# Kernel tuning notes

Hardware: AMD Instinct MI355X
Metric: run time of the kernel (lower is better)

The kernel has to match this reference:

```python
import jax, jax.numpy as jnp
import numpy as np

SEQ_LEN = 256
NLAYERS = 3
H = 128  # latent_dim == input_dim
OUT_DIM = 2
BATCH = 1024


def setup_inputs() -> dict:
    key = jax.random.key(0)
    ks = jax.random.split(key, 7)
    s = 1.0 / np.sqrt(H)  # PyTorch RNN init scale
    return {
        "hiddens": jax.random.normal(ks[0], (BATCH, NLAYERS, H), jnp.float32),
        "W_ih": jax.random.uniform(ks[1], (NLAYERS, 3 * H, H), jnp.float32, -s, s),
        "W_hh": jax.random.uniform(ks[2], (NLAYERS, 3 * H, H), jnp.float32, -s, s),
        "b_ih": jax.random.uniform(ks[3], (NLAYERS, 3 * H), jnp.float32, -s, s),
        "b_hh": jax.random.uniform(ks[4], (NLAYERS, 3 * H), jnp.float32, -s, s),
        "fc_w": jax.random.uniform(ks[5], (OUT_DIM, H), jnp.float32, -s, s),
        "fc_b": jax.random.uniform(ks[6], (OUT_DIM,), jnp.float32, -s, s),
    }


def _gru_cell(x, h, w_ih, w_hh, bi, bh):
    # x, h: [B, H]; w_*: [3H, H]; b_*: [3H]; PyTorch gate order (r, z, n)
    gx = x @ w_ih.T + bi          # [B, 3H]
    gh = h @ w_hh.T + bh          # [B, 3H]
    xr, xz, xn = jnp.split(gx, 3, axis=-1)
    hr, hz, hn = jnp.split(gh, 3, axis=-1)
    r = jax.nn.sigmoid(xr + hr)
    z = jax.nn.sigmoid(xz + hz)
    n = jnp.tanh(xn + r * hn)
    return (1.0 - z) * n + z * h


def reference(hiddens, W_ih, W_hh, b_ih, b_hh, fc_w, fc_b):
    # hiddens: [B, L, H] -> layer-major [L, B, H] (torch transposes 0,1)
    h = jnp.transpose(hiddens, (1, 0, 2))
    B = hiddens.shape[0]
    x0 = jnp.zeros((B, H), hiddens.dtype)  # torch.zeros initial input

    def step(carry, _):
        x, h = carry
        new_h = []
        inp = x
        for l in range(NLAYERS):
            hl = _gru_cell(inp, h[l], W_ih[l], W_hh[l], b_ih[l], b_hh[l])
            new_h.append(hl)
            inp = hl  # top-layer output feeds next layer / next step
        return (inp, jnp.stack(new_h)), inp

    (_, _), outs = jax.lax.scan(step, (x0, h), None, length=SEQ_LEN)
    outs = jnp.transpose(outs, (1, 0, 2))        # [B, T, H]
    return outs @ fc_w.T + fc_b                  # [B, T, out_dim]
```

## Files before the change

kernel.cpp:

```cpp
#include <hip/hip_runtime.h>
#include <stdint.h>

typedef int   v4i __attribute__((ext_vector_type(4)));
typedef float v4f __attribute__((ext_vector_type(4)));

#define SLOT_SZ  13824
#define LO_OFF   6912
#define BIAS_OFF (2*SLOT_SZ)
#define FC_OFF   (BIAS_OFF + 6144)
#define SMEM_SZ  (FC_OFF + 2048)

#define QW   1436.84056f
#define C1f  4.38394754e-5f
#define C2f  3.45193507e-7f
#define L2E  1.44269504f
#define CR1  (-(L2E)*C1f)
#define CR2  (-(L2E)*C2f)
#define CX1  (2.0f*L2E*C1f)
#define CX2  (2.0f*L2E*C2f)

#define MFMA(A,B,C) __builtin_amdgcn_mfma_i32_16x16x64_i8(A, B, C, 0, 0, 0)

__global__ void prep_weights(const float* __restrict__ Wih,
                             const float* __restrict__ Whh,
                             int8_t* __restrict__ img) {
  int bid = blockIdx.x, lane = threadIdx.x;
  int w = bid / 36, blk = bid % 36;
  int l = blk / 12, rem = blk % 12, o = rem >> 1, kh = rem & 1;
  const float* M = (o & 1) ? Whh : Wih;
  int row = (o >> 1) * 128 + w * 16 + (lane & 15);
  int k0 = kh * 64 + (lane >> 4) * 16;
  const float* src = M + l * 49152 + row * 128 + k0;
  int words[4];
  #pragma unroll
  for (int j4 = 0; j4 < 4; ++j4) {
    unsigned wd = 0;
    #pragma unroll
    for (int j = 0; j < 4; ++j) {
      int q = (int)rintf(src[j4 * 4 + j] * QW);
      wd |= ((unsigned)(q & 255)) << (8 * j);
    }
    words[j4] = (int)wd;
  }
  *(v4i*)(img + (((long)bid) * 64 + lane) * 16) = *(const v4i*)words;
}

__global__ __launch_bounds__(512, 2)
void gru_main(const float* __restrict__ hiddens, const float* __restrict__ bih,
              const float* __restrict__ bhh, const float* __restrict__ fcw,
              const float* __restrict__ fcb, const int8_t* __restrict__ img,
              float* __restrict__ out) {
  extern __shared__ char smem[];
  const int tid = threadIdx.x, wg = blockIdx.x;
  const int lane = tid & 63, w = tid >> 6, col = lane & 15, q = lane >> 4;

  v4i wr[36];
  #pragma unroll
  for (int i = 0; i < 36; ++i)
    wr[i] = *(const v4i*)(img + (((long)(w * 36 + i)) * 64 + lane) * 16);

  if (tid < 128) {
    int kh = tid >> 6, ln = tid & 63, c2 = ln & 15, q2 = ln >> 4;
    int words[4] = {0, 0, 0, 0};
    if (c2 < 2) {
      const float* src = fcw + c2 * 128 + kh * 64 + q2 * 16;
      #pragma unroll
      for (int j4 = 0; j4 < 4; ++j4) {
        unsigned wd = 0;
        #pragma unroll
        for (int j = 0; j < 4; ++j) {
          int qv = (int)rintf(src[j4 * 4 + j] * QW);
          wd |= ((unsigned)(qv & 255)) << (8 * j);
        }
        words[j4] = (int)wd;
      }
    }
    *(v4i*)(smem + FC_OFF + kh * 1024 + ln * 16) = *(const v4i*)words;
  }
  for (int i = tid; i < 1536; i += 512) {
    int l = i >> 9, type = (i >> 7) & 3, h = i & 127;
    float bv;
    if      (type == 0) bv = -L2E * (bih[l * 384 + h]       + bhh[l * 384 + h]);
    else if (type == 1) bv = -L2E * (bih[l * 384 + 128 + h] + bhh[l * 384 + 128 + h]);
    else if (type == 2) bv = 2.0f * L2E * bih[l * 384 + 256 + h];
    else                bv = 2.0f * L2E * bhh[l * 384 + 256 + h];
    *(float*)(smem + BIAS_OFF + i * 4) = bv;
  }
  for (int i = tid; i < 6144; i += 512) {
    int l = i >> 11, b = (i >> 7) & 15, h = i & 127;
    float v = hiddens[((long)(wg * 16 + b)) * 384 + l * 128 + h];
    float f = v * 15.875f, fhi = rintf(f);
    *(int8_t*)(smem + l * 2304 + b * 144 + h)          = (int8_t)(int)fhi;
    *(int8_t*)(smem + l * 2304 + b * 144 + h + LO_OFF) = (int8_t)(int)rintf((f - fhi) * 127.f);
  }
  v4f hst[3];
  #pragma unroll
  for (int l = 0; l < 3; ++l)
    #pragma unroll
    for (int r = 0; r < 4; ++r)
      hst[l][r] = hiddens[((long)(wg * 16 + col)) * 384 + l * 128 + w * 16 + q * 4 + r];

  const float fcb0 = fcb[0], fcb1 = fcb[1];
  __syncthreads();

  const char* fragb = smem + col * 144 + q * 16;
  char* ewb = smem + col * 144 + w * 16 + q * 4;
  const char* biasb = smem + BIAS_OFF + (w * 16 + q * 4) * 4;

  v4i c2h[2], c2l[2];

  #pragma unroll 1
  for (int t = 0; t < 256; ++t) {
    const int so = (t & 1) * SLOT_SZ;
    const int sn = SLOT_SZ - so;
    #pragma unroll
    for (int l = 0; l < 3; ++l) {
      v4f bRv = *(const v4f*)(biasb + (l * 4 + 0) * 512);
      v4f bZv = *(const v4f*)(biasb + (l * 4 + 1) * 512);
      v4f bXv = *(const v4f*)(biasb + (l * 4 + 2) * 512);
      v4f bHv = *(const v4f*)(biasb + (l * 4 + 3) * 512);
      v4i aRh = {0,0,0,0}, aRl = {0,0,0,0}, aZh = {0,0,0,0}, aZl = {0,0,0,0};
      v4i aXh = {0,0,0,0}, aXl = {0,0,0,0}, aHh = {0,0,0,0}, aHl = {0,0,0,0};
      if (l > 0 || t > 0) {
        #pragma unroll
        for (int kh = 0; kh < 2; ++kh) {
          v4i xh, xl;
          if (l == 0) {
            xh = *(const v4i*)(fragb + so + 2 * 2304 + kh * 64);
            xl = *(const v4i*)(fragb + so + 2 * 2304 + kh * 64 + LO_OFF);
            c2h[kh] = xh; c2l[kh] = xl;
          } else {
            xh = *(const v4i*)(fragb + sn + (l - 1) * 2304 + kh * 64);
            xl = *(const v4i*)(fragb + sn + (l - 1) * 2304 + kh * 64 + LO_OFF);
          }
          aRh = MFMA(wr[l*12 + 0 + kh], xh, aRh);
          aRl = MFMA(wr[l*12 + 0 + kh], xl, aRl);
          aZh = MFMA(wr[l*12 + 4 + kh], xh, aZh);
          aZl = MFMA(wr[l*12 + 4 + kh], xl, aZl);
          aXh = MFMA(wr[l*12 + 8 + kh], xh, aXh);
          aXl = MFMA(wr[l*12 + 8 + kh], xl, aXl);
        }
      }
      #pragma unroll
      for (int kh = 0; kh < 2; ++kh) {
        v4i hh, hl;
        if (l == 2) {
          if (t == 0) { c2h[kh] = *(const v4i*)(fragb + so + 2 * 2304 + kh * 64);
                        c2l[kh] = *(const v4i*)(fragb + so + 2 * 2304 + kh * 64 + LO_OFF); }
          hh = c2h[kh]; hl = c2l[kh];
        } else {
          hh = *(const v4i*)(fragb + so + l * 2304 + kh * 64);
          hl = *(const v4i*)(fragb + so + l * 2304 + kh * 64 + LO_OFF);
        }
        aRh = MFMA(wr[l*12 + 2 + kh], hh, aRh);
        aRl = MFMA(wr[l*12 + 2 + kh], hl, aRl);
        aZh = MFMA(wr[l*12 + 6 + kh], hh, aZh);
        aZl = MFMA(wr[l*12 + 6 + kh], hl, aZl);
        aHh = MFMA(wr[l*12 + 10 + kh], hh, aHh);
        aHl = MFMA(wr[l*12 + 10 + kh], hl, aHl);
      }
      unsigned hiw = 0, low = 0;
      #pragma unroll
      for (int r = 0; r < 4; ++r) {
        float gR = fmaf(CR1, (float)aRh[r], fmaf(CR2, (float)aRl[r], bRv[r]));
        float gZ = fmaf(CR1, (float)aZh[r], fmaf(CR2, (float)aZl[r], bZv[r]));
        float gX = fmaf(CX1, (float)aXh[r], fmaf(CX2, (float)aXl[r], bXv[r]));
        float gH = fmaf(CX1, (float)aHh[r], fmaf(CX2, (float)aHl[r], bHv[r]));
        float rg = __builtin_amdgcn_rcpf(1.f + __builtin_amdgcn_exp2f(gR));
        float zg = __builtin_amdgcn_rcpf(1.f + __builtin_amdgcn_exp2f(gZ));
        float u  = __builtin_amdgcn_rcpf(1.f + __builtin_amdgcn_exp2f(fmaf(rg, gH, gX)));
        float ng = fmaf(-2.f, u, 1.f);
        float hn = fmaf(zg, hst[l][r] - ng, ng);
        hst[l][r] = hn;
        float f = hn * 15.875f, fhi = rintf(f);
        hiw |= ((unsigned)(((int)fhi) & 255)) << (8 * r);
        low |= ((unsigned)(((int)rintf((f - fhi) * 127.f)) & 255)) << (8 * r);
      }
      *(unsigned*)(ewb + sn + l * 2304)          = hiw;
      *(unsigned*)(ewb + sn + l * 2304 + LO_OFF) = low;
      __syncthreads();
    }
    if (w == 0) {
      v4i dh = {0,0,0,0}, dl = {0,0,0,0};
      #pragma unroll
      for (int kh = 0; kh < 2; ++kh) {
        v4i xh = *(const v4i*)(fragb + sn + 2 * 2304 + kh * 64);
        v4i xl = *(const v4i*)(fragb + sn + 2 * 2304 + kh * 64 + LO_OFF);
        v4i fw = *(const v4i*)(smem + FC_OFF + kh * 1024 + lane * 16);
        dh = MFMA(fw, xh, dh);
        dl = MFMA(fw, xl, dl);
      }
      if (q == 0) {
        float2 o2;
        o2.x = fcb0 + C1f * (float)dh[0] + C2f * (float)dl[0];
        o2.y = fcb1 + C1f * (float)dh[1] + C2f * (float)dl[1];
        *(float2*)(out + (((long)(wg * 16 + col)) * 256 + t) * 2) = o2;
      }
    }
  }
}

extern "C" void kernel_launch(void* const* d_in, const int* in_sizes, int n_in,
                              void* d_out, int out_size, void* d_ws, size_t ws_size,
                              hipStream_t stream) {
  (void)in_sizes; (void)n_in; (void)out_size; (void)ws_size;
  const float* hiddens = (const float*)d_in[0];
  const float* Wih     = (const float*)d_in[1];
  const float* Whh     = (const float*)d_in[2];
  const float* bih     = (const float*)d_in[3];
  const float* bhh     = (const float*)d_in[4];
  const float* fcw     = (const float*)d_in[5];
  const float* fcb     = (const float*)d_in[6];
  int8_t* img = (int8_t*)d_ws;
  float* out = (float*)d_out;

  prep_weights<<<288, 64, 0, stream>>>(Wih, Whh, img);
  gru_main<<<64, 512, SMEM_SZ, stream>>>(hiddens, bih, bhh, fcw, fcb, img, out);
}
```

Before: 836.9 us.

## Repack GRU state smem into fragment-contiguous layout and prefetch next-layer operands

Changes the shared-memory layout of the quantized hidden-state buffers from padded row-major to a fragment-contiguous layout, so each lane reads one contiguous 16-byte chunk. The per-layer loop is manually unrolled so that operands for the next layer (and the next timestep's layer-0 state) are loaded from shared memory before the elementwise stage and barrier, hiding LDS latency. Biases and FC weights move from shared memory into registers, which removes per-step LDS loads but raises register pressure against the 2-blocks-per-CU launch bound.

```diff
diff --git a/kernel.cpp b/kernel.cpp
--- a/kernel.cpp
+++ b/kernel.cpp
@@ -4,11 +4,9 @@
 typedef int   v4i __attribute__((ext_vector_type(4)));
 typedef float v4f __attribute__((ext_vector_type(4)));
 
-#define SLOT_SZ  13824
-#define LO_OFF   6912
-#define BIAS_OFF (2*SLOT_SZ)
-#define FC_OFF   (BIAS_OFF + 6144)
-#define SMEM_SZ  (FC_OFF + 2048)
+#define SLOT_SZ  12288
+#define LO_OFF   6144
+#define SMEM_SZ  (2*SLOT_SZ)
 
 #define QW   1436.84056f
 #define C1f  4.38394754e-5f
@@ -45,6 +43,49 @@
   *(v4i*)(img + (((long)bid) * 64 + lane) * 16) = *(const v4i*)words;
 }
 
+#define DECL_ACC v4i aRh={0,0,0,0},aRl={0,0,0,0},aZh={0,0,0,0},aZl={0,0,0,0}, \
+                     aXh={0,0,0,0},aXl={0,0,0,0},aHh={0,0,0,0},aHl={0,0,0,0}
+
+#define HMFMA(L,H0,LL0,H1,LL1) do { \
+  aRh = MFMA(wr[(L)*12+2],  H0,  aRh);  aRl = MFMA(wr[(L)*12+2],  LL0, aRl); \
+  aZh = MFMA(wr[(L)*12+6],  H0,  aZh);  aZl = MFMA(wr[(L)*12+6],  LL0, aZl); \
+  aHh = MFMA(wr[(L)*12+10], H0,  aHh);  aHl = MFMA(wr[(L)*12+10], LL0, aHl); \
+  aRh = MFMA(wr[(L)*12+3],  H1,  aRh);  aRl = MFMA(wr[(L)*12+3],  LL1, aRl); \
+  aZh = MFMA(wr[(L)*12+7],  H1,  aZh);  aZl = MFMA(wr[(L)*12+7],  LL1, aZl); \
+  aHh = MFMA(wr[(L)*12+11], H1,  aHh);  aHl = MFMA(wr[(L)*12+11], LL1, aHl); \
+} while(0)
+
+#define XMFMA(L,H0,LL0,H1,LL1) do { \
+  aRh = MFMA(wr[(L)*12+0],  H0,  aRh);  aRl = MFMA(wr[(L)*12+0],  LL0, aRl); \
+  aZh = MFMA(wr[(L)*12+4],  H0,  aZh);  aZl = MFMA(wr[(L)*12+4],  LL0, aZl); \
+  aXh = MFMA(wr[(L)*12+8],  H0,  aXh);  aXl = MFMA(wr[(L)*12+8],  LL0, aXl); \
+  aRh = MFMA(wr[(L)*12+1],  H1,  aRh);  aRl = MFMA(wr[(L)*12+1],  LL1, aRl); \
+  aZh = MFMA(wr[(L)*12+5],  H1,  aZh);  aZl = MFMA(wr[(L)*12+5],  LL1, aZl); \
+  aXh = MFMA(wr[(L)*12+9],  H1,  aXh);  aXl = MFMA(wr[(L)*12+9],  LL1, aXl); \
+} while(0)
+
+#define EW_WRITE(L, SN) do { \
+  unsigned hiw = 0, low = 0; \
+  _Pragma("unroll") \
+  for (int r = 0; r < 4; ++r) { \
+    float gR = fmaf(CR1, (float)aRh[r], fmaf(CR2, (float)aRl[r], bR[L][r])); \
+    float gZ = fmaf(CR1, (float)aZh[r], fmaf(CR2, (float)aZl[r], bZ[L][r])); \
+    float gX = fmaf(CX1, (float)aXh[r], fmaf(CX2, (float)aXl[r], bX[L][r])); \
+    float gH = fmaf(CX1, (float)aHh[r], fmaf(CX2, (float)aHl[r], bH[L][r])); \
+    float rg = __builtin_amdgcn_rcpf(1.f + __builtin_amdgcn_exp2f(gR)); \
+    float zg = __builtin_amdgcn_rcpf(1.f + __builtin_amdgcn_exp2f(gZ)); \
+    float u  = __builtin_amdgcn_rcpf(1.f + __builtin_amdgcn_exp2f(fmaf(rg, gH, gX))); \
+    float ng = fmaf(-2.f, u, 1.f); \
+    float hn = fmaf(zg, hst[L][r] - ng, ng); \
+    hst[L][r] = hn; \
+    float f = hn * 15.875f, fhi = rintf(f); \
+    hiw |= ((unsigned)(((int)fhi) & 255)) << (8 * r); \
+    low |= ((unsigned)(((int)rintf((f - fhi) * 127.f)) & 255)) << (8 * r); \
+  } \
+  *(unsigned*)(ewb + (SN) + (L)*2048)          = hiw; \
+  *(unsigned*)(ewb + (SN) + (L)*2048 + LO_OFF) = low; \
+} while(0)
+
 __global__ __launch_bounds__(512, 2)
 void gru_main(const float* __restrict__ hiddens, const float* __restrict__ bih,
               const float* __restrict__ bhh, const float* __restrict__ fcw,
@@ -59,11 +100,12 @@
   for (int i = 0; i < 36; ++i)
     wr[i] = *(const v4i*)(img + (((long)(w * 36 + i)) * 64 + lane) * 16);
 
-  if (tid < 128) {
-    int kh = tid >> 6, ln = tid & 63, c2 = ln & 15, q2 = ln >> 4;
-    int words[4] = {0, 0, 0, 0};
-    if (c2 < 2) {
-      const float* src = fcw + c2 * 128 + kh * 64 + q2 * 16;
+  v4i fw0 = {0, 0, 0, 0}, fw1 = {0, 0, 0, 0};
+  if (w == 0 && col < 2) {
+    #pragma unroll
+    for (int kh = 0; kh < 2; ++kh) {
+      const float* src = fcw + col * 128 + kh * 64 + q * 16;
+      int words[4];
       #pragma unroll
       for (int j4 = 0; j4 < 4; ++j4) {
         unsigned wd = 0;
@@ -74,25 +116,36 @@
         }
         words[j4] = (int)wd;
       }
-    }
-    *(v4i*)(smem + FC_OFF + kh * 1024 + ln * 16) = *(const v4i*)words;
-  }
-  for (int i = tid; i < 1536; i += 512) {
-    int l = i >> 9, type = (i >> 7) & 3, h = i & 127;
-    float bv;
-    if      (type == 0) bv = -L2E * (bih[l * 384 + h]       + bhh[l * 384 + h]);
-    else if (type == 1) bv = -L2E * (bih[l * 384 + 128 + h] + bhh[l * 384 + 128 + h]);
-    else if (type == 2) bv = 2.0f * L2E * bih[l * 384 + 256 + h];
-    else                bv = 2.0f * L2E * bhh[l * 384 + 256 + h];
-    *(float*)(smem + BIAS_OFF + i * 4) = bv;
-  }
+      v4i tv = {words[0], words[1], words[2], words[3]};
+      if (kh == 0) fw0 = tv; else fw1 = tv;
+    }
+  }
+
+  v4f bR[3], bZ[3], bX[3], bH[3];
+  {
+    const int rowb = w * 16 + q * 4;
+    #pragma unroll
+    for (int l = 0; l < 3; ++l) {
+      #pragma unroll
+      for (int r = 0; r < 4; ++r) {
+        int idx = rowb + r;
+        bR[l][r] = -L2E * (bih[l * 384 + idx]       + bhh[l * 384 + idx]);
+        bZ[l][r] = -L2E * (bih[l * 384 + 128 + idx] + bhh[l * 384 + 128 + idx]);
+        bX[l][r] = 2.0f * L2E * bih[l * 384 + 256 + idx];
+        bH[l][r] = 2.0f * L2E * bhh[l * 384 + 256 + idx];
+      }
+    }
+  }
+
   for (int i = tid; i < 6144; i += 512) {
     int l = i >> 11, b = (i >> 7) & 15, h = i & 127;
     float v = hiddens[((long)(wg * 16 + b)) * 384 + l * 128 + h];
     float f = v * 15.875f, fhi = rintf(f);
-    *(int8_t*)(smem + l * 2304 + b * 144 + h)          = (int8_t)(int)fhi;
-    *(int8_t*)(smem + l * 2304 + b * 144 + h + LO_OFF) = (int8_t)(int)rintf((f - fhi) * 127.f);
-  }
+    int addr = l * 2048 + (h >> 4) * 256 + b * 16 + (h & 15);
+    *(int8_t*)(smem + addr)          = (int8_t)(int)fhi;
+    *(int8_t*)(smem + addr + LO_OFF) = (int8_t)(int)rintf((f - fhi) * 127.f);
+  }
+
   v4f hst[3];
   #pragma unroll
   for (int l = 0; l < 3; ++l)
@@ -103,93 +156,70 @@
   const float fcb0 = fcb[0], fcb1 = fcb[1];
   __syncthreads();
 
-  const char* fragb = smem + col * 144 + q * 16;
-  char* ewb = smem + col * 144 + w * 16 + q * 4;
-  const char* biasb = smem + BIAS_OFF + (w * 16 + q * 4) * 4;
-
-  v4i c2h[2], c2l[2];
+  const char* fragb = smem + lane * 16;
+  char* ewb = smem + w * 256 + col * 16 + q * 4;
+
+  v4i p0h = *(const v4i*)(fragb + 0);
+  v4i p0l = *(const v4i*)(fragb + 0 + LO_OFF);
+  v4i p1h = *(const v4i*)(fragb + 1024);
+  v4i p1l = *(const v4i*)(fragb + 1024 + LO_OFF);
+  v4i c2h0, c2l0, c2h1, c2l1;
+  v4i n0h, n0l, n1h, n1l, x0h, x0l, x1h, x1l;
 
   #pragma unroll 1
   for (int t = 0; t < 256; ++t) {
     const int so = (t & 1) * SLOT_SZ;
     const int sn = SLOT_SZ - so;
-    #pragma unroll
-    for (int l = 0; l < 3; ++l) {
-      v4f bRv = *(const v4f*)(biasb + (l * 4 + 0) * 512);
-      v4f bZv = *(const v4f*)(biasb + (l * 4 + 1) * 512);
-      v4f bXv = *(const v4f*)(biasb + (l * 4 + 2) * 512);
-      v4f bHv = *(const v4f*)(biasb + (l * 4 + 3) * 512);
-      v4i aRh = {0,0,0,0}, aRl = {0,0,0,0}, aZh = {0,0,0,0}, aZl = {0,0,0,0};
-      v4i aXh = {0,0,0,0}, aXl = {0,0,0,0}, aHh = {0,0,0,0}, aHl = {0,0,0,0};
-      if (l > 0 || t > 0) {
-        #pragma unroll
-        for (int kh = 0; kh < 2; ++kh) {
-          v4i xh, xl;
-          if (l == 0) {
-            xh = *(const v4i*)(fragb + so + 2 * 2304 + kh * 64);
-            xl = *(const v4i*)(fragb + so + 2 * 2304 + kh * 64 + LO_OFF);
-            c2h[kh] = xh; c2l[kh] = xl;
-          } else {
-            xh = *(const v4i*)(fragb + sn + (l - 1) * 2304 + kh * 64);
-            xl = *(const v4i*)(fragb + sn + (l - 1) * 2304 + kh * 64 + LO_OFF);
-          }
-          aRh = MFMA(wr[l*12 + 0 + kh], xh, aRh);
-          aRl = MFMA(wr[l*12 + 0 + kh], xl, aRl);
-          aZh = MFMA(wr[l*12 + 4 + kh], xh, aZh);
-          aZl = MFMA(wr[l*12 + 4 + kh], xl, aZl);
-          aXh = MFMA(wr[l*12 + 8 + kh], xh, aXh);
-          aXl = MFMA(wr[l*12 + 8 + kh], xl, aXl);
-        }
-      }
-      #pragma unroll
-      for (int kh = 0; kh < 2; ++kh) {
-        v4i hh, hl;
-        if (l == 2) {
-          if (t == 0) { c2h[kh] = *(const v4i*)(fragb + so + 2 * 2304 + kh * 64);
-                        c2l[kh] = *(const v4i*)(fragb + so + 2 * 2304 + kh * 64 + LO_OFF); }
-          hh = c2h[kh]; hl = c2l[kh];
-        } else {
-          hh = *(const v4i*)(fragb + so + l * 2304 + kh * 64);
-          hl = *(const v4i*)(fragb + so + l * 2304 + kh * 64 + LO_OFF);
-        }
-        aRh = MFMA(wr[l*12 + 2 + kh], hh, aRh);
-        aRl = MFMA(wr[l*12 + 2 + kh], hl, aRl);
-        aZh = MFMA(wr[l*12 + 6 + kh], hh, aZh);
-        aZl = MFMA(wr[l*12 + 6 + kh], hl, aZl);
-        aHh = MFMA(wr[l*12 + 10 + kh], hh, aHh);
-        aHl = MFMA(wr[l*12 + 10 + kh], hl, aHl);
-      }
-      unsigned hiw = 0, low = 0;
-      #pragma unroll
-      for (int r = 0; r < 4; ++r) {
-        float gR = fmaf(CR1, (float)aRh[r], fmaf(CR2, (float)aRl[r], bRv[r]));
-        float gZ = fmaf(CR1, (float)aZh[r], fmaf(CR2, (float)aZl[r], bZv[r]));
-        float gX = fmaf(CX1, (float)aXh[r], fmaf(CX2, (float)aXl[r], bXv[r]));
-        float gH = fmaf(CX1, (float)aHh[r], fmaf(CX2, (float)aHl[r], bHv[r]));
-        float rg = __builtin_amdgcn_rcpf(1.f + __builtin_amdgcn_exp2f(gR));
-        float zg = __builtin_amdgcn_rcpf(1.f + __builtin_amdgcn_exp2f(gZ));
-        float u  = __builtin_amdgcn_rcpf(1.f + __builtin_amdgcn_exp2f(fmaf(rg, gH, gX)));
-        float ng = fmaf(-2.f, u, 1.f);
-        float hn = fmaf(zg, hst[l][r] - ng, ng);
-        hst[l][r] = hn;
-        float f = hn * 15.875f, fhi = rintf(f);
-        hiw |= ((unsigned)(((int)fhi) & 255)) << (8 * r);
-        low |= ((unsigned)(((int)rintf((f - fhi) * 127.f)) & 255)) << (8 * r);
-      }
-      *(unsigned*)(ewb + sn + l * 2304)          = hiw;
-      *(unsigned*)(ewb + sn + l * 2304 + LO_OFF) = low;
+
+    {
+      DECL_ACC;
+      c2h0 = *(const v4i*)(fragb + so + 2 * 2048);
+      c2l0 = *(const v4i*)(fragb + so + 2 * 2048 + LO_OFF);
+      c2h1 = *(const v4i*)(fragb + so + 2 * 2048 + 1024);
+      c2l1 = *(const v4i*)(fragb + so + 2 * 2048 + 1024 + LO_OFF);
+      HMFMA(0, p0h, p0l, p1h, p1l);
+      if (t > 0) XMFMA(0, c2h0, c2l0, c2h1, c2l1);
+      n0h = *(const v4i*)(fragb + so + 2048);
+      n0l = *(const v4i*)(fragb + so + 2048 + LO_OFF);
+      n1h = *(const v4i*)(fragb + so + 2048 + 1024);
+      n1l = *(const v4i*)(fragb + so + 2048 + 1024 + LO_OFF);
+      EW_WRITE(0, sn);
       __syncthreads();
     }
+    {
+      DECL_ACC;
+      x0h = *(const v4i*)(fragb + sn + 0);
+      x0l = *(const v4i*)(fragb + sn + 0 + LO_OFF);
+      x1h = *(const v4i*)(fragb + sn + 1024);
+      x1l = *(const v4i*)(fragb + sn + 1024 + LO_OFF);
+      HMFMA(1, n0h, n0l, n1h, n1l);
+      XMFMA(1, x0h, x0l, x1h, x1l);
+      EW_WRITE(1, sn);
+      __syncthreads();
+    }
+    {
+      DECL_ACC;
+      x0h = *(const v4i*)(fragb + sn + 2048);
+      x0l = *(const v4i*)(fragb + sn + 2048 + LO_OFF);
+      x1h = *(const v4i*)(fragb + sn + 2048 + 1024);
+      x1l = *(const v4i*)(fragb + sn + 2048 + 1024 + LO_OFF);
+      HMFMA(2, c2h0, c2l0, c2h1, c2l1);
+      XMFMA(2, x0h, x0l, x1h, x1l);
+      p0h = *(const v4i*)(fragb + sn + 0);
+      p0l = *(const v4i*)(fragb + sn + 0 + LO_OFF);
+      p1h = *(const v4i*)(fragb + sn + 1024);
+      p1l = *(const v4i*)(fragb + sn + 1024 + LO_OFF);
+      EW_WRITE(2, sn);
+      __syncthreads();
+    }
     if (w == 0) {
-      v4i dh = {0,0,0,0}, dl = {0,0,0,0};
-      #pragma unroll
-      for (int kh = 0; kh < 2; ++kh) {
-        v4i xh = *(const v4i*)(fragb + sn + 2 * 2304 + kh * 64);
-        v4i xl = *(const v4i*)(fragb + sn + 2 * 2304 + kh * 64 + LO_OFF);
-        v4i fw = *(const v4i*)(smem + FC_OFF + kh * 1024 + lane * 16);
-        dh = MFMA(fw, xh, dh);
-        dl = MFMA(fw, xl, dl);
-      }
+      v4i dh = {0, 0, 0, 0}, dl = {0, 0, 0, 0};
+      v4i fh0 = *(const v4i*)(fragb + sn + 2 * 2048);
+      v4i fl0 = *(const v4i*)(fragb + sn + 2 * 2048 + LO_OFF);
+      v4i fh1 = *(const v4i*)(fragb + sn + 2 * 2048 + 1024);
+      v4i fl1 = *(const v4i*)(fragb + sn + 2 * 2048 + 1024 + LO_OFF);
+      dh = MFMA(fw0, fh0, dh);  dl = MFMA(fw0, fl0, dl);
+      dh = MFMA(fw1, fh1, dh);  dl = MFMA(fw1, fl1, dl);
       if (q == 0) {
         float2 o2;
         o2.x = fcb0 + C1f * (float)dh[0] + C2f * (float)dl[0];
```

Measured after the change: 1.099 ms. +31.3%, slower.
